# Kernel optimization log

Hardware: AMD Instinct MI355X
Metric: run time of the kernel (lower is better)

Reference implementation:

```python
import jax, jax.numpy as jnp
import numpy as np

CUTOFF = 4.0
RBF_N = 32          # distance_embedding_size == D_rbf
F_DIM = 128         # hidden_size
N_ATOMS = 20000
N_PROBES = 100000
N_EDGES = 262144
LN_EPS = 1e-5


def setup_inputs() -> dict:
    key = jax.random.key(0)
    ks = jax.random.split(key, 20)
    s = 0.02
    inp = {
        "diff_pi": jax.random.normal(ks[0], (N_EDGES, 3), jnp.float32),
        "S_JK": jax.random.normal(ks[1], (N_ATOMS, F_DIM), jnp.float32),
        "V_JK": jax.random.normal(ks[2], (N_ATOMS, 3, F_DIM), jnp.float32),
        "atom_idx": jax.random.randint(ks[3], (N_EDGES,), 0, N_ATOMS),
        "probe_idx": jax.random.randint(ks[4], (N_EDGES,), 0, N_PROBES),
        "num_probes": N_PROBES,
        # state branch params
        "w_s1": jax.random.normal(ks[5], (3 * F_DIM, F_DIM), jnp.float32) * s,
        "b_s1": jnp.zeros((F_DIM,), jnp.float32),
        "g_ln": jnp.ones((F_DIM,), jnp.float32),
        "b_ln": jnp.zeros((F_DIM,), jnp.float32),
        "w_s2": jax.random.normal(ks[6], (F_DIM, F_DIM), jnp.float32) * s,
        "b_s2": jnp.zeros((F_DIM,), jnp.float32),
        # filter branch params
        "w_f1": jax.random.normal(ks[7], (RBF_N, F_DIM), jnp.float32) * s,
        "b_f1": jnp.zeros((F_DIM,), jnp.float32),
        "w_f2": jax.random.normal(ks[8], (F_DIM, F_DIM), jnp.float32) * s,
        "b_f2": jnp.zeros((F_DIM,), jnp.float32),
        # output head params
        "w_o1": jax.random.normal(ks[9], (F_DIM, F_DIM // 2), jnp.float32) * s,
        "b_o1": jnp.zeros((F_DIM // 2,), jnp.float32),
        "w_o2": jax.random.normal(ks[10], (F_DIM // 2, 1), jnp.float32) * s,
        "b_o2": jnp.zeros((1,), jnp.float32),
        "final_bias": jnp.array([-6.1], jnp.float32),
    }
    return inp


def reference(diff_pi, S_JK, V_JK, atom_idx, probe_idx, num_probes,
              w_s1, b_s1, g_ln, b_ln, w_s2, b_s2,
              w_f1, b_f1, w_f2, b_f2,
              w_o1, b_o1, w_o2, b_o2, final_bias):
    silu = jax.nn.silu
    # edge distances
    sq = (diff_pi ** 2).sum(-1)                       # [E]
    dist = jnp.sqrt(sq)                               # [E] exact distance
    dist_safe = jnp.sqrt(sq + 1e-8)[:, None]          # [E,1]
    r_hat = diff_pi / dist_safe                       # [E,3]

    # sinc RBF expansion: sin(n*pi*d/cutoff)/d, n=1..RBF_N
    n = jnp.arange(1, RBF_N + 1, dtype=diff_pi.dtype) # [D]
    e_pi = jnp.sin(dist[:, None] * n * (jnp.pi / CUTOFF)) / dist[:, None]  # [E,D]

    # gather atom features to edges
    n_i = jnp.sqrt((V_JK ** 2).sum(1) + 1e-8)         # [N,F]
    n_e = n_i[atom_idx]                               # [E,F]
    V_e = V_JK[atom_idx]                              # [E,3,F]
    q_pi = (V_e * r_hat[:, :, None]).sum(1)           # [E,F]
    S_e = S_JK[atom_idx]                              # [E,F]

    # state branch: Linear -> LayerNorm -> SiLU -> Linear
    h = jnp.concatenate([S_e, n_e, q_pi], axis=-1)    # [E,3F]
    u = h @ w_s1 + b_s1                               # [E,F]
    mu = u.mean(-1, keepdims=True)
    var = ((u - mu) ** 2).mean(-1, keepdims=True)
    u_norm = (u - mu) / jnp.sqrt(var + LN_EPS) * g_ln + b_ln
    state = silu(u_norm) @ w_s2 + b_s2                # [E,F]

    # filter branch (no normalization -> absolute distance scale)
    W = silu(e_pi @ w_f1 + b_f1) @ w_f2 + b_f2        # [E,F]

    # fuse + output head
    m = (silu((W * state) @ w_o1 + b_o1) @ w_o2 + b_o2)[:, 0]  # [E]

    x = dist / CUTOFF
    env = 1.0 - 21.0 * x ** 5 + 35.0 * x ** 6 - 15.0 * x ** 7
    env = jnp.where(dist < CUTOFF, env, jnp.zeros_like(env))
    m_w = m * env

    # scatter-add to probes
    rho = jax.ops.segment_sum(m_w, probe_idx, num_segments=num_probes)
    return rho + final_bias[0]
```

## Files before the change

kernel.cpp:

```cpp
#include <hip/hip_runtime.h>

#define EPB     64
#define E_TOTAL 262144
#define NPROBE  100000
#define N_ATOMS 20000

#define ASTR   136
#define A2_O   0
#define F1_O   8704
#define EPI_O  17408
#define LDS_SH 19968

#define WS1_O  0
#define WS2_O  49152
#define WF1_O  65536
#define WF2_O  69632
#define WO1_O  86016
#define WT_TOT 94208
#define PQ_O   WT_TOT

typedef __attribute__((ext_vector_type(8))) short          short8;
typedef __attribute__((ext_vector_type(8))) unsigned short ushort8;
typedef __attribute__((ext_vector_type(4))) float          floatx4;

#define MFMA16(a, b, c) __builtin_amdgcn_mfma_f32_16x16x32_bf16((a), (b), (c), 0, 0, 0)

__device__ __forceinline__ short f2bf(float x) {
    unsigned u = __builtin_bit_cast(unsigned, x);
    u = (u + 0x7FFFu + ((u >> 16) & 1u)) >> 16;
    return (short)(unsigned short)u;
}
__device__ __forceinline__ unsigned pk2(float lo, float hi) {
    return __builtin_amdgcn_perm(__builtin_bit_cast(unsigned, hi),
                                 __builtin_bit_cast(unsigned, lo), 0x07060302u);
}
__device__ __forceinline__ float bf2f(unsigned short u) {
    return __builtin_bit_cast(float, ((unsigned)u) << 16);
}
__device__ __forceinline__ float silu_f(float x) { return x / (1.0f + __expf(-x)); }

struct F8 { float v[8]; };
__device__ __forceinline__ F8 ld8(const float* __restrict__ p) {
    F8 r;
    const float4 a = *(const float4*)p;
    const float4 b = *(const float4*)(p + 4);
    r.v[0] = a.x; r.v[1] = a.y; r.v[2] = a.z; r.v[3] = a.w;
    r.v[4] = b.x; r.v[5] = b.y; r.v[6] = b.z; r.v[7] = b.w;
    return r;
}

__global__ void cfr_prep_w(const float* __restrict__ w_s1, const float* __restrict__ w_s2,
                           const float* __restrict__ w_f1, const float* __restrict__ w_f2,
                           const float* __restrict__ w_o1,
                           const float* __restrict__ fb, float* __restrict__ out,
                           unsigned short* __restrict__ wt) {
    int i = blockIdx.x * 256 + threadIdx.x;
    if (i < NPROBE) out[i] = fb[0];
    if (i < WT_TOT) {
        float v;
        if (i < WS2_O)      { int n = i / 384, k = i - n * 384;          v = w_s1[k * 128 + n]; }
        else if (i < WF1_O) { int j = i - WS2_O, n = j >> 7, k = j & 127; v = w_s2[k * 128 + n]; }
        else if (i < WF2_O) { int j = i - WF1_O, n = j >> 5, k = j & 31;  v = w_f1[k * 128 + n]; }
        else if (i < WO1_O) { int j = i - WF2_O, n = j >> 7, k = j & 127; v = w_f2[k * 128 + n]; }
        else                { int j = i - WO1_O, n = j >> 7, k = j & 127; v = w_o1[k * 64 + n]; }
        wt[i] = (unsigned short)f2bf(v);
    }
}

__global__ __launch_bounds__(256, 1) void cfr_prep_pq(
    const float* __restrict__ S, const float* __restrict__ V,
    const float* __restrict__ b_s1,
    const unsigned short* __restrict__ wt, unsigned short* __restrict__ pq)
{
    __shared__ __align__(16) unsigned short bufH[64 * 264];
    __shared__ __align__(16) unsigned short bufV[192 * 136];

    const int t    = threadIdx.x;
    const int a0   = blockIdx.x * 64;
    const int wave = t >> 6;
    const int lane = t & 63;
    const int q    = lane >> 4;
    const int c16  = lane & 15;

#pragma unroll
    for (int it = 0; it < 4; ++it) {
        int idx = it * 256 + t;
        int al = idx >> 4, f8 = (idx & 15) * 8;
        int a = a0 + al;
        ushort8 sS, sN, s0, s1, s2;
        if (a < N_ATOMS) {
            F8 s  = ld8(S + a * 128 + f8);
            F8 v0 = ld8(V + a * 384 + f8);
            F8 v1 = ld8(V + a * 384 + 128 + f8);
            F8 v2 = ld8(V + a * 384 + 256 + f8);
#pragma unroll
            for (int j = 0; j < 8; ++j) {
                sS[j] = (unsigned short)f2bf(s.v[j]);
                sN[j] = (unsigned short)f2bf(sqrtf(v0.v[j]*v0.v[j] + v1.v[j]*v1.v[j] + v2.v[j]*v2.v[j] + 1e-8f));
                s0[j] = (unsigned short)f2bf(v0.v[j]);
                s1[j] = (unsigned short)f2bf(v1.v[j]);
                s2[j] = (unsigned short)f2bf(v2.v[j]);
            }
        } else {
#pragma unroll
            for (int j = 0; j < 8; ++j) { sS[j]=0; sN[j]=0; s0[j]=0; s1[j]=0; s2[j]=0; }
        }
        *(ushort8*)&bufH[al * 264 + f8]        = sS;
        *(ushort8*)&bufH[al * 264 + 128 + f8]  = sN;
        *(ushort8*)&bufV[(al) * 136 + f8]       = s0;
        *(ushort8*)&bufV[(64 + al) * 136 + f8]  = s1;
        *(ushort8*)&bufV[(128 + al) * 136 + f8] = s2;
    }
    __syncthreads();

    const floatx4 zero4 = {0.f, 0.f, 0.f, 0.f};
    float bs1c[2];
#pragma unroll
    for (int ni = 0; ni < 2; ++ni) bs1c[ni] = b_s1[wave * 32 + ni * 16 + c16];

    {
        floatx4 pacc[4][2];
#pragma unroll
        for (int mi = 0; mi < 4; ++mi) { pacc[mi][0] = zero4; pacc[mi][1] = zero4; }
#pragma unroll
        for (int kk = 0; kk < 8; ++kk) {
            short8 bfr[2], af[4];
#pragma unroll
            for (int ni = 0; ni < 2; ++ni) {
                int n = wave * 32 + ni * 16 + c16;
                bfr[ni] = *(const short8*)&wt[WS1_O + n * 384 + kk * 32 + q * 8];
            }
#pragma unroll
            for (int mi = 0; mi < 4; ++mi)
                af[mi] = *(const short8*)&bufH[(mi * 16 + c16) * 264 + kk * 32 + q * 8];
#pragma unroll
            for (int mi = 0; mi < 4; ++mi)
#pragma unroll
                for (int ni = 0; ni < 2; ++ni)
                    pacc[mi][ni] = MFMA16(af[mi], bfr[ni], pacc[mi][ni]);
        }
#pragma unroll
        for (int mi = 0; mi < 4; ++mi)
#pragma unroll
            for (int r = 0; r < 4; ++r) {
                int a = a0 + mi * 16 + q * 4 + r;
                if (a < N_ATOMS)
#pragma unroll
                    for (int ni = 0; ni < 2; ++ni) {
                        int col = wave * 32 + ni * 16 + c16;
                        pq[a * 512 + col] = (unsigned short)f2bf(pacc[mi][ni][r] + bs1c[ni]);
                    }
            }
    }

    short8 bq[4][2];
#pragma unroll
    for (int kk = 0; kk < 4; ++kk)
#pragma unroll
        for (int ni = 0; ni < 2; ++ni) {
            int n = wave * 32 + ni * 16 + c16;
            bq[kk][ni] = *(const short8*)&wt[WS1_O + n * 384 + 256 + kk * 32 + q * 8];
        }
#pragma unroll
    for (int d = 0; d < 3; ++d) {
        floatx4 qacc[4][2];
#pragma unroll
        for (int mi = 0; mi < 4; ++mi) { qacc[mi][0] = zero4; qacc[mi][1] = zero4; }
#pragma unroll
        for (int kk = 0; kk < 4; ++kk) {
            short8 af[4];
#pragma unroll
            for (int mi = 0; mi < 4; ++mi)
                af[mi] = *(const short8*)&bufV[(d * 64 + mi * 16 + c16) * 136 + kk * 32 + q * 8];
#pragma unroll
            for (int mi = 0; mi < 4; ++mi)
#pragma unroll
                for (int ni = 0; ni < 2; ++ni)
                    qacc[mi][ni] = MFMA16(af[mi], bq[kk][ni], qacc[mi][ni]);
        }
#pragma unroll
        for (int mi = 0; mi < 4; ++mi)
#pragma unroll
            for (int r = 0; r < 4; ++r) {
                int a = a0 + mi * 16 + q * 4 + r;
                if (a < N_ATOMS)
#pragma unroll
                    for (int ni = 0; ni < 2; ++ni) {
                        int col = wave * 32 + ni * 16 + c16;
                        pq[a * 512 + (1 + d) * 128 + col] = (unsigned short)f2bf(qacc[mi][ni][r]);
                    }
            }
    }
}

__global__ __launch_bounds__(256, 4) void cfr_main(
    const float* __restrict__ diff,
    const int* __restrict__ atom_idx, const int* __restrict__ probe_idx,
    const unsigned short* __restrict__ wt, const unsigned short* __restrict__ pq,
    const float* __restrict__ g_ln, const float* __restrict__ b_ln,
    const float* __restrict__ b_s2, const float* __restrict__ b_f1,
    const float* __restrict__ b_f2, const float* __restrict__ b_o1,
    const float* __restrict__ w_o2, const float* __restrict__ b_o2,
    float* __restrict__ out)
{
    __shared__ __align__(16) unsigned short LDSu[LDS_SH];
    float* mpart = (float*)&LDSu[EPI_O];

    const int t    = threadIdx.x;
    const int e0   = blockIdx.x * EPB;
    const int wave = t >> 6;
    const int lane = t & 63;
    const int q    = lane >> 4;
    const int c16  = lane & 15;
    const floatx4 zero4 = {0.f, 0.f, 0.f, 0.f};

    {
        const int el = t >> 2;
        const int c0 = (t & 3) * 32;
        const int eg = e0 + el;
        const int a  = atom_idx[eg];
        float dx = diff[eg * 3 + 0], dy = diff[eg * 3 + 1], dz = diff[eg * 3 + 2];
        float sq   = dx * dx + dy * dy + dz * dz;
        float dist = sqrtf(sq);
        float rinv = rsqrtf(sq + 1e-8f);
        float rx = dx * rinv, ry = dy * rinv, rz = dz * rinv;

        const ushort8* pqr = (const ushort8*)(pq + a * 512 + c0);
        float u[32];
#pragma unroll
        for (int g = 0; g < 4; ++g) {
            ushort8 v = pqr[g];
#pragma unroll
            for (int j = 0; j < 8; ++j) u[g * 8 + j] = bf2f(v[j]);
        }
#pragma unroll
        for (int g = 0; g < 4; ++g) {
            ushort8 v = pqr[16 + g];
#pragma unroll
            for (int j = 0; j < 8; ++j) u[g * 8 + j] = fmaf(bf2f(v[j]), rx, u[g * 8 + j]);
        }
#pragma unroll
        for (int g = 0; g < 4; ++g) {
            ushort8 v = pqr[32 + g];
#pragma unroll
            for (int j = 0; j < 8; ++j) u[g * 8 + j] = fmaf(bf2f(v[j]), ry, u[g * 8 + j]);
        }
#pragma unroll
        for (int g = 0; g < 4; ++g) {
            ushort8 v = pqr[48 + g];
#pragma unroll
            for (int j = 0; j < 8; ++j) u[g * 8 + j] = fmaf(bf2f(v[j]), rz, u[g * 8 + j]);
        }
        float s = 0.f, s2 = 0.f;
#pragma unroll
        for (int j = 0; j < 32; ++j) { s += u[j]; s2 = fmaf(u[j], u[j], s2); }
        s  += __shfl_xor(s, 1);  s  += __shfl_xor(s, 2);
        s2 += __shfl_xor(s2, 1); s2 += __shfl_xor(s2, 2);
        float mu = s * (1.f / 128.f);
        float rstd = rsqrtf(s2 * (1.f / 128.f) - mu * mu + 1e-5f);
        const float4* gp = (const float4*)(g_ln + c0);
        const float4* bp = (const float4*)(b_ln + c0);
        unsigned pko[16];
#pragma unroll
        for (int g4 = 0; g4 < 8; ++g4) {
            float4 gg = gp[g4], bb = bp[g4];
            float y0 = silu_f((u[g4 * 4 + 0] - mu) * rstd * gg.x + bb.x);
            float y1 = silu_f((u[g4 * 4 + 1] - mu) * rstd * gg.y + bb.y);
            float y2 = silu_f((u[g4 * 4 + 2] - mu) * rstd * gg.z + bb.z);
            float y3 = silu_f((u[g4 * 4 + 3] - mu) * rstd * gg.w + bb.w);
            pko[g4 * 2 + 0] = pk2(y0, y1);
            pko[g4 * 2 + 1] = pk2(y2, y3);
        }
        uint4* dst = (uint4*)&LDSu[A2_O + el * ASTR + c0];
        dst[0] = make_uint4(pko[0], pko[1], pko[2], pko[3]);
        dst[1] = make_uint4(pko[4], pko[5], pko[6], pko[7]);
        dst[2] = make_uint4(pko[8], pko[9], pko[10], pko[11]);
        dst[3] = make_uint4(pko[12], pko[13], pko[14], pko[15]);
        float inv = 1.0f / dist;
        float sv[8];
#pragma unroll
        for (int j = 0; j < 8; ++j) {
            float nf = (float)((t & 3) * 8 + j + 1);
            sv[j] = __sinf(dist * nf * 0.785398163397448f) * inv;
        }
        *(uint4*)&LDSu[EPI_O + el * 40 + (t & 3) * 8] =
            make_uint4(pk2(sv[0], sv[1]), pk2(sv[2], sv[3]), pk2(sv[4], sv[5]), pk2(sv[6], sv[7]));
    }
    __syncthreads();

    {
        short8 ae[4], be[2];
#pragma unroll
        for (int mi = 0; mi < 4; ++mi)
            ae[mi] = *(const short8*)&LDSu[EPI_O + (mi * 16 + c16) * 40 + q * 8];
#pragma unroll
        for (int ni = 0; ni < 2; ++ni) {
            int n = wave * 32 + ni * 16 + c16;
            be[ni] = *(const short8*)&wt[WF1_O + n * 32 + q * 8];
        }
        floatx4 facc[4][2];
#pragma unroll
        for (int mi = 0; mi < 4; ++mi)
#pragma unroll
            for (int ni = 0; ni < 2; ++ni)
                facc[mi][ni] = MFMA16(ae[mi], be[ni], zero4);
        float bf1c[2];
#pragma unroll
        for (int ni = 0; ni < 2; ++ni) bf1c[ni] = b_f1[wave * 32 + ni * 16 + c16];
#pragma unroll
        for (int mi = 0; mi < 4; ++mi)
#pragma unroll
            for (int r = 0; r < 4; ++r) {
                int row = mi * 16 + q * 4 + r;
#pragma unroll
                for (int ni = 0; ni < 2; ++ni) {
                    float v = facc[mi][ni][r] + bf1c[ni];
                    LDSu[F1_O + row * ASTR + (wave * 32 + ni * 16 + c16)] =
                        (unsigned short)(__builtin_bit_cast(unsigned, silu_f(v)) >> 16);
                }
            }
    }
    __syncthreads();

    {
        floatx4 sacc[4][2], wacc[4][2];
#pragma unroll
        for (int mi = 0; mi < 4; ++mi)
#pragma unroll
            for (int ni = 0; ni < 2; ++ni) { sacc[mi][ni] = zero4; wacc[mi][ni] = zero4; }
#pragma unroll
        for (int kk = 0; kk < 4; ++kk) {
            short8 a2f[4], f1f[4], b2[2], bw[2];
#pragma unroll
            for (int ni = 0; ni < 2; ++ni) {
                int n = wave * 32 + ni * 16 + c16;
                b2[ni] = *(const short8*)&wt[WS2_O + n * 128 + kk * 32 + q * 8];
                bw[ni] = *(const short8*)&wt[WF2_O + n * 128 + kk * 32 + q * 8];
            }
#pragma unroll
            for (int mi = 0; mi < 4; ++mi) {
                a2f[mi] = *(const short8*)&LDSu[A2_O + (mi * 16 + c16) * ASTR + kk * 32 + q * 8];
                f1f[mi] = *(const short8*)&LDSu[F1_O + (mi * 16 + c16) * ASTR + kk * 32 + q * 8];
            }
#pragma unroll
            for (int mi = 0; mi < 4; ++mi)
#pragma unroll
                for (int ni = 0; ni < 2; ++ni) {
                    sacc[mi][ni] = MFMA16(a2f[mi], b2[ni], sacc[mi][ni]);
                    wacc[mi][ni] = MFMA16(f1f[mi], bw[ni], wacc[mi][ni]);
                }
        }
        __syncthreads();
        float bs2c[2], bf2c[2];
#pragma unroll
        for (int ni = 0; ni < 2; ++ni) {
            int col = wave * 32 + ni * 16 + c16;
            bs2c[ni] = b_s2[col]; bf2c[ni] = b_f2[col];
        }
#pragma unroll
        for (int mi = 0; mi < 4; ++mi)
#pragma unroll
            for (int r = 0; r < 4; ++r) {
                int row = mi * 16 + q * 4 + r;
#pragma unroll
                for (int ni = 0; ni < 2; ++ni) {
                    float g = (sacc[mi][ni][r] + bs2c[ni]) * (wacc[mi][ni][r] + bf2c[ni]);
                    LDSu[A2_O + row * ASTR + (wave * 32 + ni * 16 + c16)] =
                        (unsigned short)(__builtin_bit_cast(unsigned, g) >> 16);
                }
            }
    }
    __syncthreads();

    {
        const int n2 = wave * 16 + c16;
        floatx4 oacc[4];
#pragma unroll
        for (int mi = 0; mi < 4; ++mi) oacc[mi] = zero4;
#pragma unroll
        for (int kk = 0; kk < 4; ++kk) {
            short8 bfr = *(const short8*)&wt[WO1_O + n2 * 128 + kk * 32 + q * 8];
#pragma unroll
            for (int mi = 0; mi < 4; ++mi) {
                short8 af = *(const short8*)&LDSu[A2_O + (mi * 16 + c16) * ASTR + kk * 32 + q * 8];
                oacc[mi] = MFMA16(af, bfr, oacc[mi]);
            }
        }
        float bo1c = b_o1[n2], wo2c = w_o2[n2];
#pragma unroll
        for (int mi = 0; mi < 4; ++mi)
#pragma unroll
            for (int r = 0; r < 4; ++r) {
                float s = silu_f(oacc[mi][r] + bo1c) * wo2c;
#pragma unroll
                for (int d = 1; d < 16; d <<= 1) s += __shfl_xor(s, d, 64);
                if (c16 == 0) mpart[(mi * 16 + q * 4 + r) * 4 + wave] = s;
            }
    }
    __syncthreads();

    if (t < EPB) {
        int eg = e0 + t;
        float m = mpart[t * 4 + 0] + mpart[t * 4 + 1] + mpart[t * 4 + 2] + mpart[t * 4 + 3] + b_o2[0];
        float dx = diff[eg * 3 + 0], dy = diff[eg * 3 + 1], dz = diff[eg * 3 + 2];
        float dist = sqrtf(dx * dx + dy * dy + dz * dz);
        float x  = dist * 0.25f;
        float x2 = x * x, x4 = x2 * x2;
        float x5 = x4 * x, x6 = x5 * x, x7 = x6 * x;
        float env = 1.0f - 21.0f * x5 + 35.0f * x6 - 15.0f * x7;
        env = (dist < 4.0f) ? env : 0.0f;
        float mw = m * env;
        if (mw != 0.f) unsafeAtomicAdd(&out[probe_idx[eg]], mw);
    }
}

extern "C" void kernel_launch(void* const* d_in, const int* in_sizes, int n_in,
                              void* d_out, int out_size, void* d_ws, size_t ws_size,
                              hipStream_t stream) {
    const float* diff    = (const float*)d_in[0];
    const float* S_JK    = (const float*)d_in[1];
    const float* V_JK    = (const float*)d_in[2];
    const int*   atom_i  = (const int*)d_in[3];
    const int*   probe_i = (const int*)d_in[4];
    const float* w_s1 = (const float*)d_in[6];
    const float* b_s1 = (const float*)d_in[7];
    const float* g_ln = (const float*)d_in[8];
    const float* b_ln = (const float*)d_in[9];
    const float* w_s2 = (const float*)d_in[10];
    const float* b_s2 = (const float*)d_in[11];
    const float* w_f1 = (const float*)d_in[12];
    const float* b_f1 = (const float*)d_in[13];
    const float* w_f2 = (const float*)d_in[14];
    const float* b_f2 = (const float*)d_in[15];
    const float* w_o1 = (const float*)d_in[16];
    const float* b_o1 = (const float*)d_in[17];
    const float* w_o2 = (const float*)d_in[18];
    const float* b_o2 = (const float*)d_in[19];
    const float* fbias = (const float*)d_in[20];
    float* out = (float*)d_out;

    unsigned short* wt = (unsigned short*)d_ws;
    unsigned short* pqp = wt + PQ_O;

    cfr_prep_w<<<(NPROBE + 255) / 256, 256, 0, stream>>>(w_s1, w_s2, w_f1, w_f2, w_o1,
                                                         fbias, out, wt);
    cfr_prep_pq<<<(N_ATOMS + 63) / 64, 256, 0, stream>>>(S_JK, V_JK, b_s1, wt, pqp);
    cfr_main<<<E_TOTAL / EPB, 256, 0, stream>>>(diff, atom_i, probe_i, wt, pqp,
        g_ln, b_ln, b_s2, b_f1, b_f2, b_o1, w_o2, b_o2, out);
}
```

Measured before the change: 241.0 us.

## Replace per-edge filter MLP with an interpolated distance lookup table

```diff
diff --git a/kernel.cpp b/kernel.cpp
--- a/kernel.cpp
+++ b/kernel.cpp
@@ -4,20 +4,21 @@
 #define E_TOTAL 262144
 #define NPROBE  100000
 #define N_ATOMS 20000
+#define NTAB    4096
 
 #define ASTR   136
 #define A2_O   0
-#define F1_O   8704
-#define EPI_O  17408
-#define LDS_SH 19968
+#define S_O    8704
+#define MPT_O  17408
+#define LDS_SH 17920
 
 #define WS1_O  0
 #define WS2_O  49152
-#define WF1_O  65536
-#define WF2_O  69632
-#define WO1_O  86016
-#define WT_TOT 94208
-#define PQ_O   WT_TOT
+#define WO1_O  65536
+#define WT_TOT 73728
+#define PQ_O   73728
+#define PQ_SH  (N_ATOMS * 512)
+#define WTAB_OFF_B ((PQ_O + PQ_SH) * 2)
 
 typedef __attribute__((ext_vector_type(8))) short          short8;
 typedef __attribute__((ext_vector_type(8))) unsigned short ushort8;
@@ -50,7 +51,6 @@
 }
 
 __global__ void cfr_prep_w(const float* __restrict__ w_s1, const float* __restrict__ w_s2,
-                           const float* __restrict__ w_f1, const float* __restrict__ w_f2,
                            const float* __restrict__ w_o1,
                            const float* __restrict__ fb, float* __restrict__ out,
                            unsigned short* __restrict__ wt) {
@@ -59,31 +59,50 @@
     if (i < WT_TOT) {
         float v;
         if (i < WS2_O)      { int n = i / 384, k = i - n * 384;          v = w_s1[k * 128 + n]; }
-        else if (i < WF1_O) { int j = i - WS2_O, n = j >> 7, k = j & 127; v = w_s2[k * 128 + n]; }
-        else if (i < WF2_O) { int j = i - WF1_O, n = j >> 5, k = j & 31;  v = w_f1[k * 128 + n]; }
-        else if (i < WO1_O) { int j = i - WF2_O, n = j >> 7, k = j & 127; v = w_f2[k * 128 + n]; }
+        else if (i < WO1_O) { int j = i - WS2_O, n = j >> 7, k = j & 127; v = w_s2[k * 128 + n]; }
         else                { int j = i - WO1_O, n = j >> 7, k = j & 127; v = w_o1[k * 64 + n]; }
         wt[i] = (unsigned short)f2bf(v);
     }
 }
 
-__global__ __launch_bounds__(256, 1) void cfr_prep_pq(
+__global__ __launch_bounds__(128) void cfr_prep_wtab(
+    const float* __restrict__ w_f1, const float* __restrict__ b_f1,
+    const float* __restrict__ w_f2, const float* __restrict__ b_f2,
+    float* __restrict__ wtab)
+{
+    __shared__ float ep[32];
+    __shared__ float f1s[128];
+    const int t = threadIdx.x, row = blockIdx.x;
+    float d = fmaxf(row * (4.0f / NTAB), 1e-4f);
+    if (t < 32) ep[t] = sinf(d * (t + 1) * 0.7853981633974483f) / d;
+    __syncthreads();
+    float f1 = b_f1[t];
+#pragma unroll
+    for (int k = 0; k < 32; ++k) f1 = fmaf(ep[k], w_f1[k * 128 + t], f1);
+    f1s[t] = silu_f(f1);
+    __syncthreads();
+    float w = b_f2[t];
+    for (int k = 0; k < 128; ++k) w = fmaf(f1s[k], w_f2[k * 128 + t], w);
+    wtab[row * 128 + t] = w;
+}
+
+__global__ __launch_bounds__(256, 3) void cfr_prep_pq(
     const float* __restrict__ S, const float* __restrict__ V,
     const float* __restrict__ b_s1,
     const unsigned short* __restrict__ wt, unsigned short* __restrict__ pq)
 {
-    __shared__ __align__(16) unsigned short bufH[64 * 264];
-    __shared__ __align__(16) unsigned short bufV[192 * 136];
+    __shared__ __align__(16) unsigned short bufH[32 * 264];
+    __shared__ __align__(16) unsigned short bufV[96 * 136];
 
     const int t    = threadIdx.x;
-    const int a0   = blockIdx.x * 64;
+    const int a0   = blockIdx.x * 32;
     const int wave = t >> 6;
     const int lane = t & 63;
     const int q    = lane >> 4;
     const int c16  = lane & 15;
 
 #pragma unroll
-    for (int it = 0; it < 4; ++it) {
+    for (int it = 0; it < 2; ++it) {
         int idx = it * 256 + t;
         int al = idx >> 4, f8 = (idx & 15) * 8;
         int a = a0 + al;
@@ -107,9 +126,9 @@
         }
         *(ushort8*)&bufH[al * 264 + f8]        = sS;
         *(ushort8*)&bufH[al * 264 + 128 + f8]  = sN;
-        *(ushort8*)&bufV[(al) * 136 + f8]       = s0;
-        *(ushort8*)&bufV[(64 + al) * 136 + f8]  = s1;
-        *(ushort8*)&bufV[(128 + al) * 136 + f8] = s2;
+        *(ushort8*)&bufV[al * 136 + f8]        = s0;
+        *(ushort8*)&bufV[(32 + al) * 136 + f8] = s1;
+        *(ushort8*)&bufV[(64 + al) * 136 + f8] = s2;
     }
     __syncthreads();
 
@@ -119,28 +138,28 @@
     for (int ni = 0; ni < 2; ++ni) bs1c[ni] = b_s1[wave * 32 + ni * 16 + c16];
 
     {
-        floatx4 pacc[4][2];
-#pragma unroll
-        for (int mi = 0; mi < 4; ++mi) { pacc[mi][0] = zero4; pacc[mi][1] = zero4; }
+        floatx4 pacc[2][2];
+#pragma unroll
+        for (int mi = 0; mi < 2; ++mi) { pacc[mi][0] = zero4; pacc[mi][1] = zero4; }
 #pragma unroll
         for (int kk = 0; kk < 8; ++kk) {
-            short8 bfr[2], af[4];
+            short8 bfr[2], af[2];
 #pragma unroll
             for (int ni = 0; ni < 2; ++ni) {
                 int n = wave * 32 + ni * 16 + c16;
                 bfr[ni] = *(const short8*)&wt[WS1_O + n * 384 + kk * 32 + q * 8];
             }
 #pragma unroll
-            for (int mi = 0; mi < 4; ++mi)
+            for (int mi = 0; mi < 2; ++mi)
                 af[mi] = *(const short8*)&bufH[(mi * 16 + c16) * 264 + kk * 32 + q * 8];
 #pragma unroll
-            for (int mi = 0; mi < 4; ++mi)
+            for (int mi = 0; mi < 2; ++mi)
 #pragma unroll
                 for (int ni = 0; ni < 2; ++ni)
                     pacc[mi][ni] = MFMA16(af[mi], bfr[ni], pacc[mi][ni]);
         }
 #pragma unroll
-        for (int mi = 0; mi < 4; ++mi)
+        for (int mi = 0; mi < 2; ++mi)
 #pragma unroll
             for (int r = 0; r < 4; ++r) {
                 int a = a0 + mi * 16 + q * 4 + r;
@@ -163,23 +182,23 @@
         }
 #pragma unroll
     for (int d = 0; d < 3; ++d) {
-        floatx4 qacc[4][2];
-#pragma unroll
-        for (int mi = 0; mi < 4; ++mi) { qacc[mi][0] = zero4; qacc[mi][1] = zero4; }
+        floatx4 qacc[2][2];
+#pragma unroll
+        for (int mi = 0; mi < 2; ++mi) { qacc[mi][0] = zero4; qacc[mi][1] = zero4; }
 #pragma unroll
         for (int kk = 0; kk < 4; ++kk) {
-            short8 af[4];
-#pragma unroll
-            for (int mi = 0; mi < 4; ++mi)
-                af[mi] = *(const short8*)&bufV[(d * 64 + mi * 16 + c16) * 136 + kk * 32 + q * 8];
-#pragma unroll
-            for (int mi = 0; mi < 4; ++mi)
+            short8 af[2];
+#pragma unroll
+            for (int mi = 0; mi < 2; ++mi)
+                af[mi] = *(const short8*)&bufV[(d * 32 + mi * 16 + c16) * 136 + kk * 32 + q * 8];
+#pragma unroll
+            for (int mi = 0; mi < 2; ++mi)
 #pragma unroll
                 for (int ni = 0; ni < 2; ++ni)
                     qacc[mi][ni] = MFMA16(af[mi], bq[kk][ni], qacc[mi][ni]);
         }
 #pragma unroll
-        for (int mi = 0; mi < 4; ++mi)
+        for (int mi = 0; mi < 2; ++mi)
 #pragma unroll
             for (int r = 0; r < 4; ++r) {
                 int a = a0 + mi * 16 + q * 4 + r;
@@ -197,14 +216,14 @@
     const float* __restrict__ diff,
     const int* __restrict__ atom_idx, const int* __restrict__ probe_idx,
     const unsigned short* __restrict__ wt, const unsigned short* __restrict__ pq,
+    const float* __restrict__ wtab,
     const float* __restrict__ g_ln, const float* __restrict__ b_ln,
-    const float* __restrict__ b_s2, const float* __restrict__ b_f1,
-    const float* __restrict__ b_f2, const float* __restrict__ b_o1,
+    const float* __restrict__ b_s2, const float* __restrict__ b_o1,
     const float* __restrict__ w_o2, const float* __restrict__ b_o2,
     float* __restrict__ out)
 {
     __shared__ __align__(16) unsigned short LDSu[LDS_SH];
-    float* mpart = (float*)&LDSu[EPI_O];
+    float* mpart = (float*)&LDSu[MPT_O];
 
     const int t    = threadIdx.x;
     const int e0   = blockIdx.x * EPB;
@@ -214,14 +233,16 @@
     const int c16  = lane & 15;
     const floatx4 zero4 = {0.f, 0.f, 0.f, 0.f};
 
+    const int el = t >> 2;
+    const int c0 = (t & 3) * 32;
+    float dist;
+
     {
-        const int el = t >> 2;
-        const int c0 = (t & 3) * 32;
         const int eg = e0 + el;
         const int a  = atom_idx[eg];
         float dx = diff[eg * 3 + 0], dy = diff[eg * 3 + 1], dz = diff[eg * 3 + 2];
-        float sq   = dx * dx + dy * dy + dz * dz;
-        float dist = sqrtf(sq);
+        float sq = dx * dx + dy * dy + dz * dz;
+        dist = sqrtf(sq);
         float rinv = rsqrtf(sq + 1e-8f);
         float rx = dx * rinv, ry = dy * rinv, rz = dz * rinv;
 
@@ -276,87 +297,33 @@
         dst[1] = make_uint4(pko[4], pko[5], pko[6], pko[7]);
         dst[2] = make_uint4(pko[8], pko[9], pko[10], pko[11]);
         dst[3] = make_uint4(pko[12], pko[13], pko[14], pko[15]);
-        float inv = 1.0f / dist;
-        float sv[8];
-#pragma unroll
-        for (int j = 0; j < 8; ++j) {
-            float nf = (float)((t & 3) * 8 + j + 1);
-            sv[j] = __sinf(dist * nf * 0.785398163397448f) * inv;
-        }
-        *(uint4*)&LDSu[EPI_O + el * 40 + (t & 3) * 8] =
-            make_uint4(pk2(sv[0], sv[1]), pk2(sv[2], sv[3]), pk2(sv[4], sv[5]), pk2(sv[6], sv[7]));
     }
     __syncthreads();
 
     {
-        short8 ae[4], be[2];
-#pragma unroll
-        for (int mi = 0; mi < 4; ++mi)
-            ae[mi] = *(const short8*)&LDSu[EPI_O + (mi * 16 + c16) * 40 + q * 8];
-#pragma unroll
-        for (int ni = 0; ni < 2; ++ni) {
-            int n = wave * 32 + ni * 16 + c16;
-            be[ni] = *(const short8*)&wt[WF1_O + n * 32 + q * 8];
-        }
-        floatx4 facc[4][2];
-#pragma unroll
-        for (int mi = 0; mi < 4; ++mi)
-#pragma unroll
-            for (int ni = 0; ni < 2; ++ni)
-                facc[mi][ni] = MFMA16(ae[mi], be[ni], zero4);
-        float bf1c[2];
-#pragma unroll
-        for (int ni = 0; ni < 2; ++ni) bf1c[ni] = b_f1[wave * 32 + ni * 16 + c16];
-#pragma unroll
-        for (int mi = 0; mi < 4; ++mi)
-#pragma unroll
-            for (int r = 0; r < 4; ++r) {
-                int row = mi * 16 + q * 4 + r;
-#pragma unroll
-                for (int ni = 0; ni < 2; ++ni) {
-                    float v = facc[mi][ni][r] + bf1c[ni];
-                    LDSu[F1_O + row * ASTR + (wave * 32 + ni * 16 + c16)] =
-                        (unsigned short)(__builtin_bit_cast(unsigned, silu_f(v)) >> 16);
-                }
-            }
-    }
-    __syncthreads();
-
-    {
-        floatx4 sacc[4][2], wacc[4][2];
-#pragma unroll
-        for (int mi = 0; mi < 4; ++mi)
-#pragma unroll
-            for (int ni = 0; ni < 2; ++ni) { sacc[mi][ni] = zero4; wacc[mi][ni] = zero4; }
+        floatx4 sacc[4][2];
+#pragma unroll
+        for (int mi = 0; mi < 4; ++mi) { sacc[mi][0] = zero4; sacc[mi][1] = zero4; }
 #pragma unroll
         for (int kk = 0; kk < 4; ++kk) {
-            short8 a2f[4], f1f[4], b2[2], bw[2];
+            short8 a2f[4], b2[2];
 #pragma unroll
             for (int ni = 0; ni < 2; ++ni) {
                 int n = wave * 32 + ni * 16 + c16;
                 b2[ni] = *(const short8*)&wt[WS2_O + n * 128 + kk * 32 + q * 8];
-                bw[ni] = *(const short8*)&wt[WF2_O + n * 128 + kk * 32 + q * 8];
-            }
-#pragma unroll
-            for (int mi = 0; mi < 4; ++mi) {
+            }
+#pragma unroll
+            for (int mi = 0; mi < 4; ++mi)
                 a2f[mi] = *(const short8*)&LDSu[A2_O + (mi * 16 + c16) * ASTR + kk * 32 + q * 8];
-                f1f[mi] = *(const short8*)&LDSu[F1_O + (mi * 16 + c16) * ASTR + kk * 32 + q * 8];
-            }
 #pragma unroll
             for (int mi = 0; mi < 4; ++mi)
 #pragma unroll
-                for (int ni = 0; ni < 2; ++ni) {
+                for (int ni = 0; ni < 2; ++ni)
                     sacc[mi][ni] = MFMA16(a2f[mi], b2[ni], sacc[mi][ni]);
-                    wacc[mi][ni] = MFMA16(f1f[mi], bw[ni], wacc[mi][ni]);
-                }
-        }
-        __syncthreads();
-        float bs2c[2], bf2c[2];
-#pragma unroll
-        for (int ni = 0; ni < 2; ++ni) {
-            int col = wave * 32 + ni * 16 + c16;
-            bs2c[ni] = b_s2[col]; bf2c[ni] = b_f2[col];
-        }
+        }
+        float bs2c[2];
+#pragma unroll
+        for (int ni = 0; ni < 2; ++ni) bs2c[ni] = b_s2[wave * 32 + ni * 16 + c16];
 #pragma unroll
         for (int mi = 0; mi < 4; ++mi)
 #pragma unroll
@@ -364,11 +331,46 @@
                 int row = mi * 16 + q * 4 + r;
 #pragma unroll
                 for (int ni = 0; ni < 2; ++ni) {
-                    float g = (sacc[mi][ni][r] + bs2c[ni]) * (wacc[mi][ni][r] + bf2c[ni]);
-                    LDSu[A2_O + row * ASTR + (wave * 32 + ni * 16 + c16)] =
-                        (unsigned short)(__builtin_bit_cast(unsigned, g) >> 16);
+                    float v = sacc[mi][ni][r] + bs2c[ni];
+                    LDSu[S_O + row * ASTR + (wave * 32 + ni * 16 + c16)] =
+                        (unsigned short)(__builtin_bit_cast(unsigned, v) >> 16);
                 }
             }
+    }
+    __syncthreads();
+
+    {
+        float f  = fminf(dist * (NTAB / 4.0f), (float)(NTAB - 1));
+        float fi = floorf(f);
+        int   i0 = (int)fi;
+        float fr = f - fi;
+        const float* r0 = wtab + i0 * 128 + c0;
+        const float* r1 = r0 + 128;
+        float w0[32], w1[32];
+#pragma unroll
+        for (int g4 = 0; g4 < 8; ++g4) {
+            *(float4*)&w0[g4 * 4] = *(const float4*)(r0 + g4 * 4);
+            *(float4*)&w1[g4 * 4] = *(const float4*)(r1 + g4 * 4);
+        }
+        ushort8 sv[4];
+#pragma unroll
+        for (int g = 0; g < 4; ++g)
+            sv[g] = *(const ushort8*)&LDSu[S_O + el * ASTR + c0 + g * 8];
+        unsigned pko[16];
+#pragma unroll
+        for (int p = 0; p < 16; ++p) {
+            int j0 = p * 2, j1 = p * 2 + 1;
+            float wa = fmaf(fr, w1[j0] - w0[j0], w0[j0]);
+            float wb = fmaf(fr, w1[j1] - w0[j1], w0[j1]);
+            float ga = bf2f(sv[j0 >> 3][j0 & 7]) * wa;
+            float gb = bf2f(sv[j1 >> 3][j1 & 7]) * wb;
+            pko[p] = pk2(ga, gb);
+        }
+        uint4* dst = (uint4*)&LDSu[A2_O + el * ASTR + c0];
+        dst[0] = make_uint4(pko[0], pko[1], pko[2], pko[3]);
+        dst[1] = make_uint4(pko[4], pko[5], pko[6], pko[7]);
+        dst[2] = make_uint4(pko[8], pko[9], pko[10], pko[11]);
+        dst[3] = make_uint4(pko[12], pko[13], pko[14], pko[15]);
     }
     __syncthreads();
 
@@ -403,12 +405,12 @@
         int eg = e0 + t;
         float m = mpart[t * 4 + 0] + mpart[t * 4 + 1] + mpart[t * 4 + 2] + mpart[t * 4 + 3] + b_o2[0];
         float dx = diff[eg * 3 + 0], dy = diff[eg * 3 + 1], dz = diff[eg * 3 + 2];
-        float dist = sqrtf(dx * dx + dy * dy + dz * dz);
-        float x  = dist * 0.25f;
+        float dd = sqrtf(dx * dx + dy * dy + dz * dz);
+        float x  = dd * 0.25f;
         float x2 = x * x, x4 = x2 * x2;
         float x5 = x4 * x, x6 = x5 * x, x7 = x6 * x;
         float env = 1.0f - 21.0f * x5 + 35.0f * x6 - 15.0f * x7;
-        env = (dist < 4.0f) ? env : 0.0f;
+        env = (dd < 4.0f) ? env : 0.0f;
         float mw = m * env;
         if (mw != 0.f) unsafeAtomicAdd(&out[probe_idx[eg]], mw);
     }
@@ -439,12 +441,13 @@
     const float* fbias = (const float*)d_in[20];
     float* out = (float*)d_out;
 
-    unsigned short* wt = (unsigned short*)d_ws;
+    unsigned short* wt  = (unsigned short*)d_ws;
     unsigned short* pqp = wt + PQ_O;
-
-    cfr_prep_w<<<(NPROBE + 255) / 256, 256, 0, stream>>>(w_s1, w_s2, w_f1, w_f2, w_o1,
-                                                         fbias, out, wt);
-    cfr_prep_pq<<<(N_ATOMS + 63) / 64, 256, 0, stream>>>(S_JK, V_JK, b_s1, wt, pqp);
-    cfr_main<<<E_TOTAL / EPB, 256, 0, stream>>>(diff, atom_i, probe_i, wt, pqp,
-        g_ln, b_ln, b_s2, b_f1, b_f2, b_o1, w_o2, b_o2, out);
-}
+    float* wtab = (float*)((char*)d_ws + WTAB_OFF_B);
+
+    cfr_prep_w<<<(NPROBE + 255) / 256, 256, 0, stream>>>(w_s1, w_s2, w_o1, fbias, out, wt);
+    cfr_prep_wtab<<<NTAB + 1, 128, 0, stream>>>(w_f1, b_f1, w_f2, b_f2, wtab);
+    cfr_prep_pq<<<(N_ATOMS + 31) / 32, 256, 0, stream>>>(S_JK, V_JK, b_s1, wt, pqp);
+    cfr_main<<<E_TOTAL / EPB, 256, 0, stream>>>(diff, atom_i, probe_i, wt, pqp, wtab,
+        g_ln, b_ln, b_s2, b_o1, w_o2, b_o2, out);
+}
```

Result: slower. 249.8 us (+3.6%).
